# Performance work log

Measured on AMD Instinct MI355X. Metric: run time of the kernel, lower is better.

## Reference

```python
import jax, jax.numpy as jnp
import numpy as np
import math

D_MODEL = 1024
D_INNER = 2048
D_HALF = D_INNER // 2
D_STATE = 16
D_CONV = 4
DT_RANK = 64
B_SZ = 4
L = 2048


def _dw_conv(x, w, b):
    # x: (b, l, c), w: (k, 1, c) depthwise, SAME padding
    y = jax.lax.conv_general_dilated(
        x, w, window_strides=(1,), padding='SAME',
        feature_group_count=x.shape[-1],
        dimension_numbers=('NWC', 'WIO', 'NWC'))
    return y + b


def _selective_scan(u, delta, A, Bc, Cc, D):
    # u, delta: (b, l, d); Bc, Cc: (b, l, n); A: (d, n); D: (d,)
    b, l, d = u.shape
    n = A.shape[1]

    def step(h, inp):
        d_t, u_t, B_t, C_t = inp  # (b,d), (b,d), (b,n), (b,n)
        dA = jnp.exp(d_t[..., None] * A)                     # (b,d,n)
        h = dA * h + (d_t * u_t)[..., None] * B_t[:, None, :]
        y = jnp.einsum('bdn,bn->bd', h, C_t)
        return h, y

    h0 = jnp.zeros((b, d, n), u.dtype)
    xs = (jnp.moveaxis(delta, 1, 0), jnp.moveaxis(u, 1, 0),
          jnp.moveaxis(Bc, 1, 0), jnp.moveaxis(Cc, 1, 0))
    _, ys = jax.lax.scan(step, h0, xs)                       # (l,b,d)
    return jnp.moveaxis(ys, 0, 1) + u * D


def setup_inputs() -> dict:
    key = jax.random.key(0)
    ks = jax.random.split(key, 12)
    x = jax.random.normal(ks[0], (B_SZ, L, D_MODEL), jnp.float32)
    W_in = jax.random.normal(ks[1], (D_MODEL, D_INNER), jnp.float32) * (D_MODEL ** -0.5)
    conv_x_w = jax.random.normal(ks[2], (D_CONV, 1, D_HALF), jnp.float32) * (D_CONV ** -0.5)
    conv_x_b = jnp.zeros((D_HALF,), jnp.float32)
    conv_z_w = jax.random.normal(ks[3], (D_CONV, 1, D_HALF), jnp.float32) * (D_CONV ** -0.5)
    conv_z_b = jnp.zeros((D_HALF,), jnp.float32)
    W_xdbl = jax.random.normal(ks[4], (D_HALF, DT_RANK + 2 * D_STATE), jnp.float32) * (D_HALF ** -0.5)
    dt_init_std = DT_RANK ** -0.5  # dt_scale = 1.0
    W_dt = jax.random.uniform(ks[5], (DT_RANK, D_HALF), jnp.float32, -dt_init_std, dt_init_std)
    rand_vals = jax.random.uniform(ks[6], (D_HALF,))
    dt_bias = jnp.exp(rand_vals * (math.log(0.1) - math.log(0.001)) + math.log(0.001))
    dt_bias = jnp.clip(dt_bias, 1e-4)
    inv_dt = dt_bias + jnp.log(-jnp.expm1(-dt_bias))
    D = jnp.ones((D_HALF,), jnp.float32)
    W_out = jax.random.normal(ks[7], (D_INNER, D_MODEL), jnp.float32) * (D_INNER ** -0.5)
    b_out = jnp.zeros((D_MODEL,), jnp.float32)
    return dict(x=x, W_in=W_in, conv_x_w=conv_x_w, conv_x_b=conv_x_b,
                conv_z_w=conv_z_w, conv_z_b=conv_z_b, W_xdbl=W_xdbl,
                W_dt=W_dt, inv_dt=inv_dt, D=D, W_out=W_out, b_out=b_out)


def reference(x, W_in, conv_x_w, conv_x_b, conv_z_w, conv_z_b, W_xdbl,
              W_dt, inv_dt, D, W_out, b_out):
    xz = x @ W_in                                            # (b,l,d_inner), no bias
    xs, z = jnp.split(xz, 2, axis=-1)                        # (b,l,d_half) each
    # A = -exp(log(arange(1..N))) tiled over channels
    A = -jnp.tile(jnp.arange(1, D_STATE + 1, dtype=jnp.float32), (D_HALF, 1))  # (d,n)
    xs = jax.nn.silu(_dw_conv(xs, conv_x_w, conv_x_b))
    z = jax.nn.silu(_dw_conv(z, conv_z_w, conv_z_b))
    x_dbl = xs @ W_xdbl                                      # (b,l,dt_rank+2n)
    dt_low, Bc, Cc = jnp.split(x_dbl, [DT_RANK, DT_RANK + D_STATE], axis=-1)
    dt = dt_low @ W_dt + inv_dt                              # Dense with bias_init=inv_dt
    delta = jax.nn.softplus(dt + inv_dt)                     # scan adds delta_bias=inv_dt again (faithful)
    y = _selective_scan(xs, delta, A, Bc, Cc, D)             # (b,l,d_half)
    y = jnp.concatenate([y, z], axis=-1)                     # (b,l,d_inner)
    return y @ W_out + b_out
```

## Files before the change

### kernel.cpp

```cpp
#include <hip/hip_runtime.h>
#include <hip/hip_bf16.h>
#include <math.h>

#define B_SZ 4
#define LSEQ 2048
#define DM 1024
#define DI 2048
#define DH 1024
#define DS 16
#define DTR 64
#define RTOT 96
#define MROWS (B_SZ * LSEQ)

#define NCH 32
#define CHUNK 64

#define KD 192

typedef short bf8_t __attribute__((ext_vector_type(8)));
typedef float f4_t __attribute__((ext_vector_type(4)));

__device__ __forceinline__ unsigned short f2bfbits(float v) {
  __hip_bfloat16 h = __float2bfloat16(v);
  return *(unsigned short*)&h;
}
__device__ __forceinline__ float bfu_lo(unsigned int v) {
  unsigned int x = v << 16;
  return *(float*)&x;
}
__device__ __forceinline__ float bfu_hi(unsigned int v) {
  unsigned int x = v & 0xffff0000u;
  return *(float*)&x;
}
__device__ __forceinline__ float bf16f(unsigned short h) {
  unsigned int x = ((unsigned int)h) << 16;
  return *(float*)&x;
}

__device__ __forceinline__ void gl_lds16(const void* g, void* l) {
  __builtin_amdgcn_global_load_lds(
      (const __attribute__((address_space(1))) unsigned int*)g,
      (__attribute__((address_space(3))) unsigned int*)l,
      16, 0, 0);
}
__device__ __forceinline__ void gl_lds16_nt(const void* g, void* l) {
  __builtin_amdgcn_global_load_lds(
      (const __attribute__((address_space(1))) unsigned int*)g,
      (__attribute__((address_space(3))) unsigned int*)l,
      16, 0, 2);
}

__device__ __forceinline__ void ld8f(const float* p, unsigned short* d) {
  const float4 a = ((const float4*)p)[0];
  const float4 b = ((const float4*)p)[1];
  d[0] = f2bfbits(a.x); d[1] = f2bfbits(a.y); d[2] = f2bfbits(a.z); d[3] = f2bfbits(a.w);
  d[4] = f2bfbits(b.x); d[5] = f2bfbits(b.y); d[6] = f2bfbits(b.z); d[7] = f2bfbits(b.w);
}

#define VMCNT(n) asm volatile("s_waitcnt vmcnt(" #n ")" ::: "memory")
#define LGKM0 asm volatile("s_waitcnt lgkmcnt(0)" ::: "memory")

__global__ void probe_kernel(const unsigned short* __restrict__ p, int* __restrict__ flag) {
  int lane = threadIdx.x;
  int sane = 0;
#pragma unroll
  for (int j = 0; j < 4; j++) {
    unsigned short lo = p[(lane * 4 + j) * 2];
    int e = (lo >> 7) & 0xFF;
    sane += (e <= 130) ? 1 : 0;
  }
  sane += __shfl_xor(sane, 1, 64);
  sane += __shfl_xor(sane, 2, 64);
  sane += __shfl_xor(sane, 4, 64);
  sane += __shfl_xor(sane, 8, 64);
  sane += __shfl_xor(sane, 16, 64);
  sane += __shfl_xor(sane, 32, 64);
  if (lane == 0) *flag = (sane >= 220) ? 1 : 0;
}

__global__ __launch_bounds__(256) void cast_kernel(
    const int* __restrict__ flag, const float* __restrict__ x,
    unsigned short* __restrict__ xbf) {
  if (*flag == 1) return;
  int i = (blockIdx.x * 256 + threadIdx.x) * 8;
  unsigned short d[8];
  ld8f(x + i, d);
  *(uint4*)&xbf[i] = *(uint4*)d;
}

#define PREP_TOT 78848
__global__ __launch_bounds__(256) void prep_kernel(
    const int* __restrict__ flag,
    const void* s0, const void* s1, const void* s2, const void* s3,
    const void* s4, const void* s5, const void* s6, const void* s7,
    float* __restrict__ out) {
  int i = blockIdx.x * 256 + threadIdx.x;
  if (i >= PREP_TOT) return;
  const void* src; int off;
  if      (i < 4096)   { src = s0; off = i; }
  else if (i < 5120)   { src = s1; off = i - 4096; }
  else if (i < 9216)   { src = s2; off = i - 5120; }
  else if (i < 10240)  { src = s3; off = i - 9216; }
  else if (i < 75776)  { src = s4; off = i - 10240; }
  else if (i < 76800)  { src = s5; off = i - 75776; }
  else if (i < 77824)  { src = s6; off = i - 76800; }
  else                 { src = s7; off = i - 77824; }
  float v = (*flag == 1) ? __bfloat162float(((const __hip_bfloat16*)src)[off])
                         : ((const float*)src)[off];
  out[i] = v;
}

__global__ __launch_bounds__(256) void transpose_kernel(
    const int* __restrict__ flag, const void* __restrict__ W,
    unsigned short* __restrict__ Wt, int K, int N) {
  __shared__ unsigned short tile[32][33];
  int n0 = blockIdx.x * 32, k0 = blockIdx.y * 32;
  int c = threadIdx.x & 31, r8 = threadIdx.x >> 5;
  bool isbf = (*flag == 1);
#pragma unroll
  for (int p = 0; p < 4; p++) {
    int r = r8 + p * 8;
    unsigned short v;
    if (isbf) v = ((const unsigned short*)W)[(size_t)(k0 + r) * N + n0 + c];
    else      v = f2bfbits(((const float*)W)[(size_t)(k0 + r) * N + n0 + c]);
    tile[r][c] = v;
  }
  __syncthreads();
#pragma unroll
  for (int p = 0; p < 4; p++) {
    int r = r8 + p * 8;
    Wt[(size_t)(n0 + r) * K + k0 + c] = tile[c][r];
  }
}

__global__ __launch_bounds__(256) void transpose_pad_kernel(
    const int* __restrict__ flag, const void* __restrict__ W,
    unsigned short* __restrict__ Wt) {
  __shared__ unsigned short tile[32][33];
  int n0 = blockIdx.x * 32, k0 = blockIdx.y * 32;
  int c = threadIdx.x & 31, r8 = threadIdx.x >> 5;
  bool isbf = (*flag == 1);
#pragma unroll
  for (int p = 0; p < 4; p++) {
    int r = r8 + p * 8;
    unsigned short v = 0;
    if (n0 + c < RTOT) {
      if (isbf) v = ((const unsigned short*)W)[(size_t)(k0 + r) * RTOT + n0 + c];
      else      v = f2bfbits(((const float*)W)[(size_t)(k0 + r) * RTOT + n0 + c]);
    }
    tile[r][c] = v;
  }
  __syncthreads();
#pragma unroll
  for (int p = 0; p < 4; p++) {
    int r = r8 + p * 8;
    Wt[(size_t)(n0 + r) * DH + k0 + c] = tile[c][r];
  }
}

__global__ __launch_bounds__(256) void wdtt_kernel(
    const float* __restrict__ Wdt, unsigned short* __restrict__ Wdtt) {
  __shared__ unsigned short th[32][33], tl[32][33];
  int n0 = blockIdx.x * 32, k0 = blockIdx.y * 32;
  int c = threadIdx.x & 31, r8 = threadIdx.x >> 5;
#pragma unroll
  for (int p = 0; p < 4; p++) {
    int r = r8 + p * 8;
    float w = Wdt[(size_t)(k0 + r) * DH + n0 + c];
    unsigned short hi = f2bfbits(w);
    th[r][c] = hi;
    tl[r][c] = f2bfbits(w - bf16f(hi));
  }
  __syncthreads();
#pragma unroll
  for (int p = 0; p < 4; p++) {
    int r = r8 + p * 8;
    unsigned short hi = th[c][r], lo = tl[c][r];
    size_t base = (size_t)(n0 + r) * KD + k0 + c;
    Wdtt[base] = hi;
    Wdtt[base + 64] = hi;
    Wdtt[base + 128] = lo;
  }
}

template <int BN, bool OUT_BY_FLAG>
__global__ __launch_bounds__(512, 2) void gemm_bk32(
    const int* __restrict__ flag,
    const unsigned short* __restrict__ A1, const unsigned short* __restrict__ A0,
    const unsigned short* __restrict__ Bt,
    const float* __restrict__ bias, void* __restrict__ C,
    int N, int K) {
  extern __shared__ __align__(16) unsigned short lds[];
  constexpr int A_BUF = 256 * 32;
  constexpr int B_BUF = BN * 32;
  constexpr int B_OFF = 4 * A_BUF;
  constexpr int NF = BN / 64;
  constexpr int NB_LD = BN / 128;

  const int flagv = *flag;
  const unsigned short* Ap = (flagv == 1) ? A1 : A0;

  const int tid = threadIdx.x;
  const int lane = tid & 63;
  const int wave = tid >> 6;
  const int quad = lane >> 4;
  const int l16 = lane & 15;
  const int wm = wave >> 2;
  const int wn = wave & 3;

  const int NB = gridDim.x, MB = gridDim.y;
  int L = blockIdx.y * NB + blockIdx.x;
  int xcd = L & 7;
  int w = L >> 3;
  int m_band = xcd * (MB >> 3) + (w / NB);
  int n_blk = w % NB;
  const int m0 = m_band * 256;
  const int n0 = n_blk * BN;

  const int NT = K >> 5;

  f4_t acc[8][NF] = {};

  auto stage = [&](int kt) {
    const int buf = kt & 3;
    const int k0 = kt * 32;
    unsigned short* Ad = lds + buf * A_BUF;
#pragma unroll
    for (int j = 0; j < 2; j++) {
      int ch = tid + j * 512;
      int mi = ch >> 2, s = ch & 3;
      int ki = s ^ ((mi >> 1) & 3);
      gl_lds16_nt(Ap + (size_t)(m0 + mi) * K + k0 + ki * 8,
                  Ad + (j * 512 + wave * 64) * 8);
    }
    unsigned short* Bd = lds + B_OFF + buf * B_BUF;
#pragma unroll
    for (int j = 0; j < NB_LD; j++) {
      int ch = tid + j * 512;
      int ni = ch >> 2, s = ch & 3;
      int ki = s ^ ((ni >> 1) & 3);
      gl_lds16(Bt + (size_t)(n0 + ni) * K + k0 + ki * 8,
               Bd + (j * 512 + wave * 64) * 8);
    }
  };

  stage(0); stage(1); stage(2);

  for (int t = 0; t < NT; t++) {
    if (t + 2 < NT) {
      if constexpr (NF == 4) VMCNT(8); else VMCNT(6);
    } else if (t + 1 < NT) {
      if constexpr (NF == 4) VMCNT(4); else VMCNT(3);
    } else {
      VMCNT(0);
    }
    __builtin_amdgcn_s_barrier();

    const unsigned short* Ac = lds + (t & 3) * A_BUF;
    const unsigned short* Bc = lds + B_OFF + (t & 3) * B_BUF;
    bf8_t af[8], bfr[NF];
#pragma unroll
    for (int ti = 0; ti < 8; ti++) {
      int r = wm * 128 + ti * 16 + l16;
      af[ti] = *(const bf8_t*)&Ac[(r * 4 + (quad ^ ((r >> 1) & 3))) * 8];
    }
#pragma unroll
    for (int tj = 0; tj < NF; tj++) {
      int rn = wn * (BN / 4) + tj * 16 + l16;
      bfr[tj] = *(const bf8_t*)&Bc[(rn * 4 + (quad ^ ((rn >> 1) & 3))) * 8];
    }
    if (t + 3 < NT) stage(t + 3);

    LGKM0;
    __builtin_amdgcn_sched_barrier(0);
    __builtin_amdgcn_s_setprio(1);
#pragma unroll
    for (int ti = 0; ti < 8; ti++)
#pragma unroll
      for (int tj = 0; tj < NF; tj++)
        acc[ti][tj] = __builtin_amdgcn_mfma_f32_16x16x32_bf16(
            af[ti], bfr[tj], acc[ti][tj], 0, 0, 0);
    __builtin_amdgcn_s_setprio(0);
    __builtin_amdgcn_s_barrier();
  }

#pragma unroll
  for (int ti = 0; ti < 8; ti++) {
#pragma unroll
    for (int tj = 0; tj < NF; tj++) {
      int col = n0 + wn * (BN / 4) + tj * 16 + l16;
      float bv = bias ? bias[col] : 0.f;
#pragma unroll
      for (int r = 0; r < 4; r++) {
        int row = m0 + wm * 128 + ti * 16 + quad * 4 + r;
        float v = acc[ti][tj][r] + bv;
        if constexpr (!OUT_BY_FLAG) {
          __builtin_nontemporal_store(f2bfbits(v),
              (unsigned short*)C + (size_t)row * N + col);
        } else {
          if (flagv == 1)
            __builtin_nontemporal_store(f2bfbits(v),
                (unsigned short*)C + (size_t)row * N + col);
          else
            __builtin_nontemporal_store(v, (float*)C + (size_t)row * N + col);
        }
      }
    }
  }
}

__global__ __launch_bounds__(256) void xdbl_kernel(
    const unsigned short* __restrict__ A, const unsigned short* __restrict__ Bt,
    float* __restrict__ xdbl, unsigned short* __restrict__ Adelta) {
  const int tid = threadIdx.x;
  const int wave = tid >> 6;
  const int lane = tid & 63;
  const int quad = lane >> 4;
  const int l16 = lane & 15;
  const int m0 = blockIdx.x * 32 + (wave & 1) * 16;
  const int c0 = (wave >> 1) * 48;

  f4_t acc[3] = {};
  const unsigned short* Ar = A + (size_t)(m0 + l16) * DH + quad * 8;
  const unsigned short* B0 = Bt + (size_t)(c0 + l16) * DH + quad * 8;
  const unsigned short* B1 = Bt + (size_t)(c0 + 16 + l16) * DH + quad * 8;
  const unsigned short* B2 = Bt + (size_t)(c0 + 32 + l16) * DH + quad * 8;

#pragma unroll 4
  for (int k0 = 0; k0 < DH; k0 += 32) {
    bf8_t af = *(const bf8_t*)(Ar + k0);
    bf8_t b0 = *(const bf8_t*)(B0 + k0);
    bf8_t b1 = *(const bf8_t*)(B1 + k0);
    bf8_t b2 = *(const bf8_t*)(B2 + k0);
    acc[0] = __builtin_amdgcn_mfma_f32_16x16x32_bf16(af, b0, acc[0], 0, 0, 0);
    acc[1] = __builtin_amdgcn_mfma_f32_16x16x32_bf16(af, b1, acc[1], 0, 0, 0);
    acc[2] = __builtin_amdgcn_mfma_f32_16x16x32_bf16(af, b2, acc[2], 0, 0, 0);
  }

#pragma unroll
  for (int tj = 0; tj < 3; tj++) {
    int col = c0 + tj * 16 + l16;
#pragma unroll
    for (int r = 0; r < 4; r++) {
      int row = m0 + quad * 4 + r;
      float v = acc[tj][r];
      if (col < 64) {
        unsigned short hi = f2bfbits(v);
        unsigned short lo = f2bfbits(v - bf16f(hi));
        size_t base = (size_t)row * KD + col;
        Adelta[base] = hi;
        Adelta[base + 64] = lo;
        Adelta[base + 128] = hi;
      } else {
        xdbl[(size_t)row * RTOT + col] = v;
      }
    }
  }
}

__global__ __launch_bounds__(256) void delta_mfma_kernel(
    const unsigned short* __restrict__ Ad,
    const unsigned short* __restrict__ Bd,
    const float* __restrict__ inv_dt,
    const unsigned short* __restrict__ xs,
    unsigned int* __restrict__ du) {
  const int tid = threadIdx.x;
  const int wave = tid >> 6;
  const int lane = tid & 63;
  const int quad = lane >> 4;
  const int l16 = lane & 15;
  const int m0 = blockIdx.x * 128 + wave * 32;
  const int n0 = blockIdx.y * 128;

  f4_t acc[2][8] = {};
  const unsigned short* Ar0 = Ad + (size_t)(m0 + l16) * KD + quad * 8;
  const unsigned short* Ar1 = Ad + (size_t)(m0 + 16 + l16) * KD + quad * 8;

#pragma unroll
  for (int ks = 0; ks < 6; ks++) {
    const int k0 = ks * 32;
    bf8_t a0 = *(const bf8_t*)(Ar0 + k0);
    bf8_t a1 = *(const bf8_t*)(Ar1 + k0);
#pragma unroll
    for (int nj = 0; nj < 8; nj++) {
      bf8_t b = *(const bf8_t*)(Bd + (size_t)(n0 + nj * 16 + l16) * KD + quad * 8 + k0);
      acc[0][nj] = __builtin_amdgcn_mfma_f32_16x16x32_bf16(a0, b, acc[0][nj], 0, 0, 0);
      acc[1][nj] = __builtin_amdgcn_mfma_f32_16x16x32_bf16(a1, b, acc[1][nj], 0, 0, 0);
    }
  }

#pragma unroll
  for (int mi = 0; mi < 2; mi++) {
#pragma unroll
    for (int nj = 0; nj < 8; nj++) {
      int col = n0 + nj * 16 + l16;
      float bias2 = 2.f * inv_dt[col];
#pragma unroll
      for (int r = 0; r < 4; r++) {
        int row = m0 + mi * 16 + quad * 4 + r;
        float v = acc[mi][nj][r] + bias2;
        float sp = (v > 0.f) ? (v + __logf(1.f + __expf(-v)))
                             : __logf(1.f + __expf(v));
        unsigned int lo = f2bfbits(sp);
        unsigned int hi = xs[(size_t)row * DH + col];
        du[(size_t)row * DH + col] = lo | (hi << 16);
      }
    }
  }
}

__global__ __launch_bounds__(256) void conv_silu_kernel(
    const unsigned short* __restrict__ xz,
    const float* __restrict__ wx, const float* __restrict__ bx,
    const float* __restrict__ wz, const float* __restrict__ bz,
    unsigned short* __restrict__ xs_bf, unsigned short* __restrict__ cat) {
  int gid = blockIdx.x * 256 + threadIdx.x;
  int cg = gid & 127;
  int c0 = cg * 8;
  int m = gid >> 7;
  int t = m & (LSEQ - 1);
  float ax[8], az[8];
#pragma unroll
  for (int i = 0; i < 8; i++) { ax[i] = bx[c0 + i]; az[i] = bz[c0 + i]; }
#pragma unroll
  for (int j = 0; j < 4; j++) {
    int tt = t - 1 + j;
    if (tt < 0 || tt >= LSEQ) continue;
    size_t row = (size_t)(m - t + tt);
    uint4 vx = *(const uint4*)&xz[row * DI + c0];
    uint4 vz = *(const uint4*)&xz[row * DI + DH + c0];
    const unsigned int* px = (const unsigned int*)&vx;
    const unsigned int* pz = (const unsigned int*)&vz;
#pragma unroll
    for (int q = 0; q < 4; q++) {
      float x0 = bfu_lo(px[q]), x1 = bfu_hi(px[q]);
      float z0 = bfu_lo(pz[q]), z1 = bfu_hi(pz[q]);
      ax[q * 2]     = fmaf(wx[j * DH + c0 + q * 2], x0, ax[q * 2]);
      ax[q * 2 + 1] = fmaf(wx[j * DH + c0 + q * 2 + 1], x1, ax[q * 2 + 1]);
      az[q * 2]     = fmaf(wz[j * DH + c0 + q * 2], z0, az[q * 2]);
      az[q * 2 + 1] = fmaf(wz[j * DH + c0 + q * 2 + 1], z1, az[q * 2 + 1]);
    }
  }
  unsigned short sx[8], sz[8];
#pragma unroll
  for (int i = 0; i < 8; i++) {
    float vx = ax[i] / (1.f + __expf(-ax[i]));
    float vz = az[i] / (1.f + __expf(-az[i]));
    sx[i] = f2bfbits(vx);
    sz[i] = f2bfbits(vz);
  }
  *(uint4*)&xs_bf[(size_t)m * DH + c0] = *(uint4*)sx;
  *(uint4*)&cat[(size_t)m * DI + DH + c0] = *(uint4*)sz;
}

__global__ __launch_bounds__(256) void scan_pass1(
    const unsigned int* __restrict__ du, const float* __restrict__ xdbl,
    float* __restrict__ Echunks, float* __restrict__ hp) {
  const int tid = threadIdx.x;
  const int d = blockIdx.x * 256 + tid;
  const int c = blockIdx.y, b = blockIdx.z;
  const int row0 = b * LSEQ + c * CHUNK;
  __shared__ float sBC[CHUNK][32];
#pragma unroll
  for (int i = 0; i < 2; i++) {
    int task = tid + i * 256;
    int r = task >> 3, seg = task & 7;
    *(float4*)&sBC[r][seg * 4] =
        *(const float4*)&xdbl[(size_t)(row0 + r) * RTOT + DTR + seg * 4];
  }
  __syncthreads();
  float h[16];
#pragma unroll
  for (int n = 0; n < 16; n++) h[n] = 0.f;
  float E = 1.f;
  for (int t = 0; t < CHUNK; t++) {
    unsigned int v = du[(size_t)(row0 + t) * DH + d];
    float dt = bfu_lo(v), ut = bfu_hi(v);
    float e = __expf(-dt);
    E *= e;
    float dv = dt * ut;
    float p = 1.f;
#pragma unroll
    for (int n = 0; n < 16; n++) {
      p *= e;
      h[n] = fmaf(p, h[n], dv * sBC[t][n]);
    }
  }
  Echunks[((size_t)c * B_SZ + b) * DH + d] = E;
#pragma unroll
  for (int n = 0; n < 16; n++)
    hp[(((size_t)c * B_SZ + b) * 16 + n) * DH + d] = h[n];
}

__global__ __launch_bounds__(256) void scan_pass2(
    const float* __restrict__ Echunks, const float* __restrict__ hp,
    float* __restrict__ hs) {
  int t = blockIdx.x * 256 + threadIdx.x;
  int d = t & 1023;
  int n = (t >> 10) & 15;
  int b = t >> 14;
  float h = 0.f;
  const int k0 = n + 1;
  for (int c = 0; c < NCH; c++) {
    float E = Echunks[((size_t)c * B_SZ + b) * DH + d];
    float a = 1.f, base = E;
    int k = k0;
#pragma unroll
    for (int i = 0; i < 5; i++) {
      if (k & 1) a *= base;
      base *= base;
      k >>= 1;
    }
    size_t idx = (((size_t)c * B_SZ + b) * 16 + n) * DH + d;
    hs[idx] = h;
    h = fmaf(a, h, hp[idx]);
  }
}

__global__ __launch_bounds__(256) void scan_pass3(
    const unsigned int* __restrict__ du, const float* __restrict__ xdbl,
    const float* __restrict__ hs, const float* __restrict__ Dvec,
    __hip_bfloat16* __restrict__ cat) {
  const int tid = threadIdx.x;
  const int d = blockIdx.x * 256 + tid;
  const int c = blockIdx.y, b = blockIdx.z;
  const int row0 = b * LSEQ + c * CHUNK;
  __shared__ float sBC[CHUNK][32];
#pragma unroll
  for (int i = 0; i < 2; i++) {
    int task = tid + i * 256;
    int r = task >> 3, seg = task & 7;
    *(float4*)&sBC[r][seg * 4] =
        *(const float4*)&xdbl[(size_t)(row0 + r) * RTOT + DTR + seg * 4];
  }
  __syncthreads();
  float h[16];
#pragma unroll
  for (int n = 0; n < 16; n++)
    h[n] = hs[(((size_t)c * B_SZ + b) * 16 + n) * DH + d];
  const float Dd = Dvec[d];
  for (int t = 0; t < CHUNK; t++) {
    unsigned int v = du[(size_t)(row0 + t) * DH + d];
    float dt = bfu_lo(v), ut = bfu_hi(v);
    float e = __expf(-dt);
    float dv = dt * ut;
    float p = 1.f, y = 0.f;
#pragma unroll
    for (int n = 0; n < 16; n++) {
      p *= e;
      h[n] = fmaf(p, h[n], dv * sBC[t][n]);
      y = fmaf(h[n], sBC[t][16 + n], y);
    }
    y = fmaf(ut, Dd, y);
    cat[(size_t)(row0 + t) * DI + d] = __float2bfloat16(y);
  }
}

extern "C" void kernel_launch(void* const* d_in, const int* in_sizes, int n_in,
                              void* d_out, int out_size, void* d_ws, size_t ws_size,
                              hipStream_t stream) {
  char* ws = (char*)d_ws;
  __hip_bfloat16* xz  = (__hip_bfloat16*)(ws);
  unsigned int* du    = (unsigned int*)(ws);
  __hip_bfloat16* xs  = (__hip_bfloat16*)(ws + ((size_t)32 << 20));
  unsigned short* xbf = (unsigned short*)(ws + ((size_t)48 << 20));
  __hip_bfloat16* cat = (__hip_bfloat16*)(ws + ((size_t)64 << 20));
  float* xdbl         = (float*)(ws + ((size_t)96 << 20));
  float* Echunks      = (float*)(ws + ((size_t)99 << 20));
  float* hp           = (float*)(ws + ((size_t)100 << 20));
  unsigned short* Wdtt = (unsigned short*)(ws + ((size_t)100 << 20));
  float* hs           = (float*)(ws + ((size_t)108 << 20));
  unsigned short* Adelta = (unsigned short*)(ws + ((size_t)108 << 20));
  unsigned short* Wt_in  = (unsigned short*)(ws + ((size_t)116 << 20));
  unsigned short* Wt_out = (unsigned short*)(ws + ((size_t)120 << 20));
  unsigned short* Wxt    = (unsigned short*)(ws + ((size_t)124 << 20));
  float* cw           = (float*)(ws + ((size_t)125 << 20));
  int* flag           = (int*)(ws + ((size_t)126 << 20));

  const float* conv_xwf = cw + 0;
  const float* conv_xbf = cw + 4096;
  const float* conv_zwf = cw + 5120;
  const float* conv_zbf = cw + 9216;
  const float* Wdtf     = cw + 10240;
  const float* inv_dtf  = cw + 75776;
  const float* Df       = cw + 76800;
  const float* b_outf   = cw + 77824;

  (void)hipFuncSetAttribute(reinterpret_cast<const void*>(&gemm_bk32<256, false>),
                            hipFuncAttributeMaxDynamicSharedMemorySize, 131072);
  (void)hipFuncSetAttribute(reinterpret_cast<const void*>(&gemm_bk32<128, true>),
                            hipFuncAttributeMaxDynamicSharedMemorySize, 98304);

  probe_kernel<<<1, 64, 0, stream>>>((const unsigned short*)d_in[0], flag);
  cast_kernel<<<4096, 256, 0, stream>>>(flag, (const float*)d_in[0], xbf);
  prep_kernel<<<(PREP_TOT + 255) / 256, 256, 0, stream>>>(
      flag, d_in[2], d_in[3], d_in[4], d_in[5], d_in[7], d_in[8], d_in[9],
      d_in[11], cw);
  transpose_kernel<<<dim3(DI / 32, DM / 32), 256, 0, stream>>>(
      flag, d_in[1], Wt_in, DM, DI);
  transpose_kernel<<<dim3(DM / 32, DI / 32), 256, 0, stream>>>(
      flag, d_in[10], Wt_out, DI, DM);
  transpose_pad_kernel<<<dim3(4, DH / 32), 256, 0, stream>>>(flag, d_in[6], Wxt);
  wdtt_kernel<<<dim3(DH / 32, 2), 256, 0, stream>>>(Wdtf, Wdtt);

  gemm_bk32<256, false><<<dim3(DI / 256, MROWS / 256), 512, 131072, stream>>>(
      flag, (const unsigned short*)d_in[0], xbf, Wt_in,
      (const float*)nullptr, xz, DI, DM);
  conv_silu_kernel<<<(MROWS * 128) / 256, 256, 0, stream>>>(
      (const unsigned short*)xz, conv_xwf, conv_xbf, conv_zwf, conv_zbf,
      (unsigned short*)xs, (unsigned short*)cat);
  xdbl_kernel<<<MROWS / 32, 256, 0, stream>>>(
      (const unsigned short*)xs, Wxt, xdbl, Adelta);
  delta_mfma_kernel<<<dim3(MROWS / 128, DH / 128), 256, 0, stream>>>(
      Adelta, Wdtt, inv_dtf, (const unsigned short*)xs, du);
  scan_pass1<<<dim3(4, NCH, B_SZ), 256, 0, stream>>>(du, xdbl, Echunks, hp);
  scan_pass2<<<256, 256, 0, stream>>>(Echunks, hp, hs);
  scan_pass3<<<dim3(4, NCH, B_SZ), 256, 0, stream>>>(du, xdbl, hs, Df, cat);
  gemm_bk32<128, true><<<dim3(DM / 128, MROWS / 256), 512, 98304, stream>>>(
      flag, (const unsigned short*)cat, (const unsigned short*)cat, Wt_out,
      b_outf, d_out, DM, DI);
}
```

Baseline: 364.6 us.

## Template GEMM on BM/BN, drop XCD remap, and register-block conv over 4 rows

The GEMM kernel now takes the M tile size as a template parameter. The output projection moves from 256x128 tiles to 128x256 tiles. The XCD-aware block remapping is removed in favour of plain blockIdx indexing. The depthwise conv+SiLU kernel now computes 4 consecutive timesteps per thread, keeps conv weights in registers and reuses overlapping input rows, so global reads drop and there are 4x fewer threads. The tradeoffs are possible L2 locality loss from the removed remap and higher register pressure in the conv kernel.

Measured after the change: 408.6 us. +12.1%, slower.

```diff
diff --git a/kernel.cpp b/kernel.cpp
--- a/kernel.cpp
+++ b/kernel.cpp
@@ -183,19 +183,22 @@
   }
 }
 
-template <int BN, bool OUT_BY_FLAG>
-__global__ __launch_bounds__(512, 2) void gemm_bk32(
+template <int BM, int BN, bool OUT_BY_FLAG>
+__global__ __launch_bounds__(512, 2) void gemm_tpl(
     const int* __restrict__ flag,
     const unsigned short* __restrict__ A1, const unsigned short* __restrict__ A0,
     const unsigned short* __restrict__ Bt,
     const float* __restrict__ bias, void* __restrict__ C,
     int N, int K) {
   extern __shared__ __align__(16) unsigned short lds[];
-  constexpr int A_BUF = 256 * 32;
+  constexpr int A_BUF = BM * 32;
   constexpr int B_BUF = BN * 32;
   constexpr int B_OFF = 4 * A_BUF;
+  constexpr int MF = BM / 32;
   constexpr int NF = BN / 64;
-  constexpr int NB_LD = BN / 128;
+  constexpr int AI = BM / 128;
+  constexpr int BI = BN / 128;
+  constexpr int LPT = AI + BI;
 
   const int flagv = *flag;
   const unsigned short* Ap = (flagv == 1) ? A1 : A0;
@@ -208,25 +211,19 @@
   const int wm = wave >> 2;
   const int wn = wave & 3;
 
-  const int NB = gridDim.x, MB = gridDim.y;
-  int L = blockIdx.y * NB + blockIdx.x;
-  int xcd = L & 7;
-  int w = L >> 3;
-  int m_band = xcd * (MB >> 3) + (w / NB);
-  int n_blk = w % NB;
-  const int m0 = m_band * 256;
-  const int n0 = n_blk * BN;
+  const int m0 = blockIdx.y * BM;
+  const int n0 = blockIdx.x * BN;
 
   const int NT = K >> 5;
 
-  f4_t acc[8][NF] = {};
+  f4_t acc[MF][NF] = {};
 
   auto stage = [&](int kt) {
     const int buf = kt & 3;
     const int k0 = kt * 32;
     unsigned short* Ad = lds + buf * A_BUF;
 #pragma unroll
-    for (int j = 0; j < 2; j++) {
+    for (int j = 0; j < AI; j++) {
       int ch = tid + j * 512;
       int mi = ch >> 2, s = ch & 3;
       int ki = s ^ ((mi >> 1) & 3);
@@ -235,7 +232,7 @@
     }
     unsigned short* Bd = lds + B_OFF + buf * B_BUF;
 #pragma unroll
-    for (int j = 0; j < NB_LD; j++) {
+    for (int j = 0; j < BI; j++) {
       int ch = tid + j * 512;
       int ni = ch >> 2, s = ch & 3;
       int ki = s ^ ((ni >> 1) & 3);
@@ -248,9 +245,9 @@
 
   for (int t = 0; t < NT; t++) {
     if (t + 2 < NT) {
-      if constexpr (NF == 4) VMCNT(8); else VMCNT(6);
+      if constexpr (LPT == 4) VMCNT(8); else VMCNT(6);
     } else if (t + 1 < NT) {
-      if constexpr (NF == 4) VMCNT(4); else VMCNT(3);
+      if constexpr (LPT == 4) VMCNT(4); else VMCNT(3);
     } else {
       VMCNT(0);
     }
@@ -258,10 +255,10 @@
 
     const unsigned short* Ac = lds + (t & 3) * A_BUF;
     const unsigned short* Bc = lds + B_OFF + (t & 3) * B_BUF;
-    bf8_t af[8], bfr[NF];
-#pragma unroll
-    for (int ti = 0; ti < 8; ti++) {
-      int r = wm * 128 + ti * 16 + l16;
+    bf8_t af[MF], bfr[NF];
+#pragma unroll
+    for (int ti = 0; ti < MF; ti++) {
+      int r = wm * (BM / 2) + ti * 16 + l16;
       af[ti] = *(const bf8_t*)&Ac[(r * 4 + (quad ^ ((r >> 1) & 3))) * 8];
     }
 #pragma unroll
@@ -275,7 +272,7 @@
     __builtin_amdgcn_sched_barrier(0);
     __builtin_amdgcn_s_setprio(1);
 #pragma unroll
-    for (int ti = 0; ti < 8; ti++)
+    for (int ti = 0; ti < MF; ti++)
 #pragma unroll
       for (int tj = 0; tj < NF; tj++)
         acc[ti][tj] = __builtin_amdgcn_mfma_f32_16x16x32_bf16(
@@ -285,14 +282,14 @@
   }
 
 #pragma unroll
-  for (int ti = 0; ti < 8; ti++) {
+  for (int ti = 0; ti < MF; ti++) {
 #pragma unroll
     for (int tj = 0; tj < NF; tj++) {
       int col = n0 + wn * (BN / 4) + tj * 16 + l16;
       float bv = bias ? bias[col] : 0.f;
 #pragma unroll
       for (int r = 0; r < 4; r++) {
-        int row = m0 + wm * 128 + ti * 16 + quad * 4 + r;
+        int row = m0 + wm * (BM / 2) + ti * 16 + quad * 4 + r;
         float v = acc[ti][tj][r] + bv;
         if constexpr (!OUT_BY_FLAG) {
           __builtin_nontemporal_store(f2bfbits(v),
@@ -417,40 +414,67 @@
   int gid = blockIdx.x * 256 + threadIdx.x;
   int cg = gid & 127;
   int c0 = cg * 8;
-  int m = gid >> 7;
-  int t = m & (LSEQ - 1);
-  float ax[8], az[8];
-#pragma unroll
-  for (int i = 0; i < 8; i++) { ax[i] = bx[c0 + i]; az[i] = bz[c0 + i]; }
+  int g = gid >> 7;
+  int m0 = g * 4;
+  int t0 = m0 & (LSEQ - 1);
+  int mbase = m0 - t0;
+
+  float wxr[4][8], wzr[4][8];
 #pragma unroll
   for (int j = 0; j < 4; j++) {
-    int tt = t - 1 + j;
+    *(float4*)&wxr[j][0] = *(const float4*)&wx[j * DH + c0];
+    *(float4*)&wxr[j][4] = *(const float4*)&wx[j * DH + c0 + 4];
+    *(float4*)&wzr[j][0] = *(const float4*)&wz[j * DH + c0];
+    *(float4*)&wzr[j][4] = *(const float4*)&wz[j * DH + c0 + 4];
+  }
+
+  float ax[4][8], az[4][8];
+#pragma unroll
+  for (int o = 0; o < 4; o++)
+#pragma unroll
+    for (int i = 0; i < 8; i++) { ax[o][i] = bx[c0 + i]; az[o][i] = bz[c0 + i]; }
+
+#pragma unroll
+  for (int rr = 0; rr < 7; rr++) {
+    int tt = t0 - 1 + rr;
     if (tt < 0 || tt >= LSEQ) continue;
-    size_t row = (size_t)(m - t + tt);
+    size_t row = (size_t)(mbase + tt);
     uint4 vx = *(const uint4*)&xz[row * DI + c0];
     uint4 vz = *(const uint4*)&xz[row * DI + DH + c0];
     const unsigned int* px = (const unsigned int*)&vx;
     const unsigned int* pz = (const unsigned int*)&vz;
+    float xv[8], zv[8];
 #pragma unroll
     for (int q = 0; q < 4; q++) {
-      float x0 = bfu_lo(px[q]), x1 = bfu_hi(px[q]);
-      float z0 = bfu_lo(pz[q]), z1 = bfu_hi(pz[q]);
-      ax[q * 2]     = fmaf(wx[j * DH + c0 + q * 2], x0, ax[q * 2]);
-      ax[q * 2 + 1] = fmaf(wx[j * DH + c0 + q * 2 + 1], x1, ax[q * 2 + 1]);
-      az[q * 2]     = fmaf(wz[j * DH + c0 + q * 2], z0, az[q * 2]);
-      az[q * 2 + 1] = fmaf(wz[j * DH + c0 + q * 2 + 1], z1, az[q * 2 + 1]);
-    }
-  }
-  unsigned short sx[8], sz[8];
-#pragma unroll
-  for (int i = 0; i < 8; i++) {
-    float vx = ax[i] / (1.f + __expf(-ax[i]));
-    float vz = az[i] / (1.f + __expf(-az[i]));
-    sx[i] = f2bfbits(vx);
-    sz[i] = f2bfbits(vz);
-  }
-  *(uint4*)&xs_bf[(size_t)m * DH + c0] = *(uint4*)sx;
-  *(uint4*)&cat[(size_t)m * DI + DH + c0] = *(uint4*)sz;
+      xv[q * 2] = bfu_lo(px[q]); xv[q * 2 + 1] = bfu_hi(px[q]);
+      zv[q * 2] = bfu_lo(pz[q]); zv[q * 2 + 1] = bfu_hi(pz[q]);
+    }
+#pragma unroll
+    for (int o = 0; o < 4; o++) {
+      int j = rr - o;
+      if (j < 0 || j > 3) continue;
+#pragma unroll
+      for (int i = 0; i < 8; i++) {
+        ax[o][i] = fmaf(wxr[j][i], xv[i], ax[o][i]);
+        az[o][i] = fmaf(wzr[j][i], zv[i], az[o][i]);
+      }
+    }
+  }
+
+#pragma unroll
+  for (int o = 0; o < 4; o++) {
+    unsigned short sx[8], sz[8];
+#pragma unroll
+    for (int i = 0; i < 8; i++) {
+      float vx = ax[o][i] / (1.f + __expf(-ax[o][i]));
+      float vz = az[o][i] / (1.f + __expf(-az[o][i]));
+      sx[i] = f2bfbits(vx);
+      sz[i] = f2bfbits(vz);
+    }
+    size_t m = (size_t)(m0 + o);
+    *(uint4*)&xs_bf[m * DH + c0] = *(uint4*)sx;
+    *(uint4*)&cat[m * DI + DH + c0] = *(uint4*)sz;
+  }
 }
 
 __global__ __launch_bounds__(256) void scan_pass1(
@@ -586,9 +610,9 @@
   const float* Df       = cw + 76800;
   const float* b_outf   = cw + 77824;
 
-  (void)hipFuncSetAttribute(reinterpret_cast<const void*>(&gemm_bk32<256, false>),
+  (void)hipFuncSetAttribute(reinterpret_cast<const void*>(&gemm_tpl<256, 256, false>),
                             hipFuncAttributeMaxDynamicSharedMemorySize, 131072);
-  (void)hipFuncSetAttribute(reinterpret_cast<const void*>(&gemm_bk32<128, true>),
+  (void)hipFuncSetAttribute(reinterpret_cast<const void*>(&gemm_tpl<128, 256, true>),
                             hipFuncAttributeMaxDynamicSharedMemorySize, 98304);
 
   probe_kernel<<<1, 64, 0, stream>>>((const unsigned short*)d_in[0], flag);
@@ -603,10 +627,10 @@
   transpose_pad_kernel<<<dim3(4, DH / 32), 256, 0, stream>>>(flag, d_in[6], Wxt);
   wdtt_kernel<<<dim3(DH / 32, 2), 256, 0, stream>>>(Wdtf, Wdtt);
 
-  gemm_bk32<256, false><<<dim3(DI / 256, MROWS / 256), 512, 131072, stream>>>(
+  gemm_tpl<256, 256, false><<<dim3(DI / 256, MROWS / 256), 512, 131072, stream>>>(
       flag, (const unsigned short*)d_in[0], xbf, Wt_in,
       (const float*)nullptr, xz, DI, DM);
-  conv_silu_kernel<<<(MROWS * 128) / 256, 256, 0, stream>>>(
+  conv_silu_kernel<<<(MROWS / 4) * 128 / 256, 256, 0, stream>>>(
       (const unsigned short*)xz, conv_xwf, conv_xbf, conv_zwf, conv_zbf,
       (unsigned short*)xs, (unsigned short*)cat);
   xdbl_kernel<<<MROWS / 32, 256, 0, stream>>>(
@@ -616,7 +640,7 @@
   scan_pass1<<<dim3(4, NCH, B_SZ), 256, 0, stream>>>(du, xdbl, Echunks, hp);
   scan_pass2<<<256, 256, 0, stream>>>(Echunks, hp, hs);
   scan_pass3<<<dim3(4, NCH, B_SZ), 256, 0, stream>>>(du, xdbl, hs, Df, cat);
-  gemm_bk32<128, true><<<dim3(DM / 128, MROWS / 256), 512, 98304, stream>>>(
+  gemm_tpl<128, 256, true><<<dim3(DM / 256, MROWS / 128), 512, 98304, stream>>>(
       flag, (const unsigned short*)cat, (const unsigned short*)cat, Wt_out,
       b_outf, d_out, DM, DI);
 }
```
